# Kernel optimization log

Measured on AMD Instinct MI355X. Metric: run time of the kernel, lower is better.

Reference implementation:

```python
import jax, jax.numpy as jnp
import numpy as np

B, N, C = 4, 32768, 256
H, M = 8, 32
D = C // H


def _uni(k, shape, scale):
    return jax.random.uniform(k, shape, jnp.float32, -scale, scale)


def setup_inputs() -> dict:
    key = jax.random.key(0)
    ks = jax.random.split(key, 17)
    kc = 1.0 / np.sqrt(C).astype(np.float32)
    km = 1.0 / np.sqrt(H * M).astype(np.float32)
    inp = {}
    inp["x"] = jax.random.normal(ks[0], (B, N, C), jnp.float32)
    inp["latent_q"] = jax.random.normal(ks[1], (C, M), jnp.float32) * 0.1
    # k_proj ResidualMLP (num_layers=2)
    inp["k_fc1_w"] = _uni(ks[2], (C, C), kc); inp["k_fc1_b"] = _uni(ks[3], (C,), kc)
    inp["k_fcs_w"] = _uni(ks[4], (2, C, C), kc); inp["k_fcs_b"] = _uni(ks[5], (2, C), kc)
    inp["k_fc2_w"] = _uni(ks[6], (C, C), kc); inp["k_fc2_b"] = _uni(ks[7], (C,), kc)
    # v_proj ResidualMLP
    inp["v_fc1_w"] = _uni(ks[8], (C, C), kc); inp["v_fc1_b"] = _uni(ks[9], (C,), kc)
    inp["v_fcs_w"] = _uni(ks[10], (2, C, C), kc); inp["v_fcs_b"] = _uni(ks[11], (2, C), kc)
    inp["v_fc2_w"] = _uni(ks[12], (C, C), kc); inp["v_fc2_b"] = _uni(ks[13], (C,), kc)
    # head-cluster mixing 1x1 conv weight (H*M, H*M)
    inp["mix_w"] = _uni(ks[14], (H * M, H * M), km)
    inp["out_w"] = _uni(ks[15], (C, C), kc); inp["out_b"] = _uni(ks[16], (C,), kc)
    return inp


def _gelu(x):
    return jax.nn.gelu(x, approximate=False)  # torch nn.GELU default (erf)


def _rmlp(x, w1, b1, ws, bs, w2, b2):
    # ResidualMLP with input_residual=output_residual=True, num_layers=2
    h = x + _gelu(x @ w1.T + b1)
    for i in range(2):
        h = h + _gelu(h @ ws[i].T + bs[i])
    return h + (h @ w2.T + b2)


def reference(x, latent_q, k_fc1_w, k_fc1_b, k_fcs_w, k_fcs_b, k_fc2_w, k_fc2_b,
              v_fc1_w, v_fc1_b, v_fcs_w, v_fcs_b, v_fc2_w, v_fc2_b,
              mix_w, out_w, out_b):
    b, n, c = x.shape
    q = latent_q.reshape(H, M, D)                       # (C, M) -> (H, M, D)
    k = _rmlp(x, k_fc1_w, k_fc1_b, k_fcs_w, k_fcs_b, k_fc2_w, k_fc2_b)
    v = _rmlp(x, v_fc1_w, v_fc1_b, v_fcs_w, v_fcs_b, v_fc2_w, v_fc2_b)
    k = k.reshape(b, n, H, D).transpose(0, 2, 1, 3)     # b h n d
    v = v.reshape(b, n, H, D).transpose(0, 2, 1, 3)     # b h n d
    scores = jnp.einsum('hmd,bhnd->bhmn', q, k)         # (B,H,M,N)
    # 1x1 conv across flattened (H*M) channels == dense mix over head-cluster dim
    mixed = jnp.einsum('pq,bqn->bpn', mix_w, scores.reshape(b, H * M, n))
    mixed = mixed.reshape(b, H, M, n)
    enc = jax.nn.softmax(mixed, axis=-1)                # over N
    dec = jax.nn.softmax(mixed, axis=-2)                # over M
    z = jnp.einsum('bhmn,bhnd->bhmd', enc, v)           # encode to clusters
    o = jnp.einsum('bhmd,bhmn->bhnd', z, dec)           # decode to points
    o = o.transpose(0, 2, 1, 3).reshape(b, n, c)
    return o @ out_w.T + out_b
```

## Files before the change

### kernel.cpp

```cpp
#include <hip/hip_runtime.h>
#include <hip/hip_bf16.h>
#include <math.h>

#define BF16 __hip_bfloat16

typedef __bf16 bf16x8 __attribute__((ext_vector_type(8)));
typedef float  f32x4  __attribute__((ext_vector_type(4)));
typedef float  f32x16 __attribute__((ext_vector_type(16)));
typedef int    i32x4  __attribute__((ext_vector_type(4)));

__device__ inline float gelu_erf(float x) {
  float xs = x * 0.70710678118654752f;
  float a = fabsf(xs);
  float t = __builtin_amdgcn_rcpf(1.0f + 0.3275911f * a);
  float p = 1.061405429f;
  p = p * t - 1.453152027f;
  p = p * t + 1.421413741f;
  p = p * t - 0.284496736f;
  p = p * t + 0.254829592f;
  float e = __expf(-a * a);
  float y = 1.0f - p * t * e;
  float s = copysignf(y, xs);
  return 0.5f * x * (1.0f + s);
}

__device__ inline bf16x8 asbf8(i32x4 v) { union { i32x4 i; bf16x8 b; } u; u.i = v; return u.b; }

__device__ inline i32x4 aload16(const char* p) {
  i32x4 d;
  asm volatile("global_load_dwordx4 %0, %1, off" : "=v"(d) : "v"(p));
  return d;
}

template <int N> __device__ inline void vmwait() {
  if constexpr (N == 0)      asm volatile("s_waitcnt vmcnt(0)" ::: "memory");
  else if constexpr (N == 4) asm volatile("s_waitcnt vmcnt(4)" ::: "memory");
  else                       asm volatile("s_waitcnt vmcnt(8)" ::: "memory");
  __builtin_amdgcn_sched_barrier(0);
}

__device__ inline f32x4 ntload4(const float* p) {
  return __builtin_nontemporal_load((const f32x4*)p);
}
__device__ inline void ntstore4(float* p, f32x4 v) {
  __builtin_nontemporal_store(v, (f32x4*)p);
}

struct WPtrs { const float* p[9]; };
struct FArgs { const BF16* w[5]; const float* b[5]; };

__global__ void cast_w_kernel(WPtrs wp, BF16* __restrict__ out) {
  int i = blockIdx.x * 256 + threadIdx.x;
  int seg = i >> 16, d = i & 65535;
  int e = d & 7, lane = (d >> 3) & 63, kt = (d >> 9) & 7;
  int nc = (d >> 12) & 3, wc = (d >> 14) & 3;
  int fr = lane & 15, fq = lane >> 4;
  int row = wc * 64 + nc * 16 + fr, col = kt * 32 + fq * 8 + e;
  out[i] = __float2bfloat16(wp.p[seg][row * 256 + col]);
}

__global__ void build_wtilde(const float* __restrict__ mixw, const float* __restrict__ lq,
                             BF16* __restrict__ wt) {
  int p = blockIdx.x, c = threadIdx.x;
  int h = c >> 5, d = c & 31;
  float s = 0.f;
#pragma unroll
  for (int j = 0; j < 32; ++j)
    s += mixw[p * 256 + h * 32 + j] * lq[(h * 32 + j) * 32 + d];
  int wc = p >> 6, nc = (p >> 4) & 3, fr = p & 15;
  int kt = c >> 5, fq = (c >> 3) & 3, e = c & 7;
  int dst = ((((wc * 4 + nc) * 8 + kt) * 64) + (fq * 16 + fr)) * 8 + e;
  wt[dst] = __float2bfloat16(s);
}

__device__ inline void issue4(i32x4 (&buf)[4], const char* wlane, int kt) {
#pragma unroll
  for (int nc = 0; nc < 4; ++nc)
    buf[nc] = aload16(wlane + (nc * 8 + kt) * 1024);
}

__device__ inline void loada4(bf16x8 (&dst)[4], const char* act, int kt, int fr, int fq) {
#pragma unroll
  for (int nr = 0; nr < 4; ++nr) {
    int r = nr * 16 + fr;
    dst[nr] = *(const bf16x8*)(act + r * 512 + ((kt * 64 + fq * 16) ^ ((r & 7) << 4)));
  }
}

__device__ inline void mfma16w(f32x4 (&acc)[4][4], const i32x4 (&wbuf)[4], const bf16x8 (&af)[4]) {
#pragma unroll
  for (int nr = 0; nr < 4; ++nr)
#pragma unroll
    for (int nc = 0; nc < 4; ++nc)
      acc[nr][nc] = __builtin_amdgcn_mfma_f32_16x16x32_bf16(asbf8(wbuf[nc]), af[nr], acc[nr][nc], 0, 0, 0);
}

__device__ inline void kloop8(f32x4 (&acc)[4][4], const char* wlane, const char* act,
                              int fr, int fq) {
  i32x4 wb0[4], wb1[4], wb2[4];
  bf16x8 afA[4], afB[4];
  issue4(wb0, wlane, 0);
  issue4(wb1, wlane, 1);
  loada4(afA, act, 0, fr, fq);
  issue4(wb2, wlane, 2); loada4(afB, act, 1, fr, fq);
  vmwait<8>(); mfma16w(acc, wb0, afA);
  issue4(wb0, wlane, 3); loada4(afA, act, 2, fr, fq);
  vmwait<8>(); mfma16w(acc, wb1, afB);
  issue4(wb1, wlane, 4); loada4(afB, act, 3, fr, fq);
  vmwait<8>(); mfma16w(acc, wb2, afA);
  issue4(wb2, wlane, 5); loada4(afA, act, 4, fr, fq);
  vmwait<8>(); mfma16w(acc, wb0, afB);
  issue4(wb0, wlane, 6); loada4(afB, act, 5, fr, fq);
  vmwait<8>(); mfma16w(acc, wb1, afA);
  issue4(wb1, wlane, 7); loada4(afA, act, 6, fr, fq);
  vmwait<8>(); mfma16w(acc, wb2, afB);
  loada4(afB, act, 7, fr, fq);
  vmwait<4>(); mfma16w(acc, wb0, afA);
  vmwait<0>(); mfma16w(acc, wb1, afB);
}

__global__ __launch_bounds__(256, 3) void fused_k_mixed(
    const float* __restrict__ xin, FArgs args,
    float* __restrict__ mixed,
    float* __restrict__ pm, float* __restrict__ ps) {
  __shared__ __align__(16) char act[64 * 512];
  const int tid = threadIdx.x;
  const int blk = blockIdx.x;
  const int wc = tid >> 6, lane = tid & 63;
  const int fr = lane & 15, fq = lane >> 4;
  const size_t row0 = (size_t)blk * 64;

  {
    const float* xg = xin + row0 * 256;
#pragma unroll
    for (int rep = 0; rep < 16; ++rep) {
      int i = rep * 256 + tid;
      int r = i >> 6, c4 = (i & 63) << 2;
      f32x4 v = ntload4(xg + r * 256 + c4);
      union { __bf16 h[4]; unsigned long long u; } p;
      p.h[0] = (__bf16)v[0]; p.h[1] = (__bf16)v[1];
      p.h[2] = (__bf16)v[2]; p.h[3] = (__bf16)v[3];
      int byte = r * 512 + ((c4 * 2) ^ ((r & 7) << 4));
      *(unsigned long long*)(act + byte) = p.u;
    }
  }
  __syncthreads();

#pragma unroll 1
  for (int L = 0; L < 5; ++L) {
    const char* wlane = (const char*)args.w[L] + (size_t)(wc * 2048 + lane) * 16;
    f32x4 acc[4][4];
#pragma unroll
    for (int nr = 0; nr < 4; ++nr)
#pragma unroll
      for (int nc = 0; nc < 4; ++nc)
#pragma unroll
        for (int j = 0; j < 4; ++j) acc[nr][nc][j] = 0.f;

    kloop8(acc, wlane, act, fr, fq);
    __syncthreads();

    if (L == 4) {
      float* mg = mixed + row0 * 256;
#pragma unroll
      for (int nc = 0; nc < 4; ++nc) {
#pragma unroll
        for (int nr = 0; nr < 4; ++nr) {
          f32x4 st = { acc[nr][nc][0], acc[nr][nc][1], acc[nr][nc][2], acc[nr][nc][3] };
          ntstore4(mg + (size_t)(nr * 16 + fr) * 256 + wc * 64 + nc * 16 + fq * 4, st);
        }
        float mx[4], sm[4];
#pragma unroll
        for (int jj = 0; jj < 4; ++jj) {
          float m0 = fmaxf(fmaxf(acc[0][nc][jj], acc[1][nc][jj]),
                           fmaxf(acc[2][nc][jj], acc[3][nc][jj]));
#pragma unroll
          for (int d = 1; d < 16; d <<= 1) m0 = fmaxf(m0, __shfl_xor(m0, d));
          float s0 = 0.f;
#pragma unroll
          for (int nr = 0; nr < 4; ++nr) s0 += __expf(acc[nr][nc][jj] - m0);
#pragma unroll
          for (int d = 1; d < 16; d <<= 1) s0 += __shfl_xor(s0, d);
          mx[jj] = m0; sm[jj] = s0;
        }
        if (fr == 0) {
          int col = wc * 64 + nc * 16 + fq * 4;
          *(float4*)(pm + (size_t)blk * 256 + col) = {mx[0], mx[1], mx[2], mx[3]};
          *(float4*)(ps + (size_t)blk * 256 + col) = {sm[0], sm[1], sm[2], sm[3]};
        }
      }
    } else {
      const float* bb = args.b[L];
#pragma unroll
      for (int nc = 0; nc < 4; ++nc) {
        float4 b4 = *(const float4*)(bb + wc * 64 + nc * 16 + fq * 4);
#pragma unroll
        for (int nr = 0; nr < 4; ++nr) {
          int r = nr * 16 + fr;
          int cb2 = wc * 128 + nc * 32 + fq * 8;
          int byte = r * 512 + (cb2 ^ ((r & 7) << 4));
          union { __bf16 h[4]; unsigned long long u; } res, w2;
          res.u = *(unsigned long long*)(act + byte);
          float o0 = acc[nr][nc][0] + b4.x;
          float o1 = acc[nr][nc][1] + b4.y;
          float o2 = acc[nr][nc][2] + b4.z;
          float o3 = acc[nr][nc][3] + b4.w;
          if (L < 3) { o0 = gelu_erf(o0); o1 = gelu_erf(o1);
                       o2 = gelu_erf(o2); o3 = gelu_erf(o3); }
          w2.h[0] = (__bf16)((float)res.h[0] + o0);
          w2.h[1] = (__bf16)((float)res.h[1] + o1);
          w2.h[2] = (__bf16)((float)res.h[2] + o2);
          w2.h[3] = (__bf16)((float)res.h[3] + o3);
          *(unsigned long long*)(act + byte) = w2.u;
        }
      }
      __syncthreads();
    }
  }
}

__global__ void softmax_merge(const float* __restrict__ pm, const float* __restrict__ ps,
                              float* __restrict__ Mf, float* __restrict__ Sf) {
  int b = blockIdx.x, t = threadIdx.x;
  const float* pmb = pm + (size_t)b * 512 * 256;
  const float* psb = ps + (size_t)b * 512 * 256;
  float m = -3.0e38f, s = 0.f;
  for (int c = 0; c < 512; ++c) {
    float m2 = pmb[c * 256 + t];
    float s2 = psb[c * 256 + t];
    float mn = fmaxf(m, m2);
    s = s * __expf(m - mn) + s2 * __expf(m2 - mn);
    m = mn;
  }
  Mf[b * 256 + t] = m;
  Sf[b * 256 + t] = 1.f / s;
}

__global__ __launch_bounds__(256, 3) void fused_v_z(
    const float* __restrict__ xin, FArgs args,
    const float* __restrict__ mixed, const float* __restrict__ Mf,
    BF16* __restrict__ zpart) {
  __shared__ __align__(16) char act[64 * 512];
  const int tid = threadIdx.x;
  const int blk = blockIdx.x;
  const int wc = tid >> 6, lane = tid & 63;
  const int fr = lane & 15, fq = lane >> 4;
  const size_t row0 = (size_t)blk * 64;

  {
    const float* xg = xin + row0 * 256;
#pragma unroll
    for (int rep = 0; rep < 16; ++rep) {
      int i = rep * 256 + tid;
      int r = i >> 6, c4 = (i & 63) << 2;
      f32x4 v = ntload4(xg + r * 256 + c4);
      union { __bf16 h[4]; unsigned long long u; } p;
      p.h[0] = (__bf16)v[0]; p.h[1] = (__bf16)v[1];
      p.h[2] = (__bf16)v[2]; p.h[3] = (__bf16)v[3];
      int byte = r * 512 + ((c4 * 2) ^ ((r & 7) << 4));
      *(unsigned long long*)(act + byte) = p.u;
    }
  }
  __syncthreads();

#pragma unroll 1
  for (int L = 0; L < 4; ++L) {
    const char* wlane = (const char*)args.w[L] + (size_t)(wc * 2048 + lane) * 16;
    f32x4 acc[4][4];
#pragma unroll
    for (int nr = 0; nr < 4; ++nr)
#pragma unroll
      for (int nc = 0; nc < 4; ++nc)
#pragma unroll
        for (int j = 0; j < 4; ++j) acc[nr][nc][j] = 0.f;

    kloop8(acc, wlane, act, fr, fq);
    __syncthreads();

    const float* bb = args.b[L];
#pragma unroll
    for (int nc = 0; nc < 4; ++nc) {
      float4 b4 = *(const float4*)(bb + wc * 64 + nc * 16 + fq * 4);
#pragma unroll
      for (int nr = 0; nr < 4; ++nr) {
        int r = nr * 16 + fr;
        int cb2 = wc * 128 + nc * 32 + fq * 8;
        int byte = r * 512 + (cb2 ^ ((r & 7) << 4));
        union { __bf16 h[4]; unsigned long long u; } res, w2;
        res.u = *(unsigned long long*)(act + byte);
        float o0 = acc[nr][nc][0] + b4.x;
        float o1 = acc[nr][nc][1] + b4.y;
        float o2 = acc[nr][nc][2] + b4.z;
        float o3 = acc[nr][nc][3] + b4.w;
        if (L < 3) { o0 = gelu_erf(o0); o1 = gelu_erf(o1);
                     o2 = gelu_erf(o2); o3 = gelu_erf(o3); }
        w2.h[0] = (__bf16)((float)res.h[0] + o0);
        w2.h[1] = (__bf16)((float)res.h[1] + o1);
        w2.h[2] = (__bf16)((float)res.h[2] + o2);
        w2.h[3] = (__bf16)((float)res.h[3] + o3);
        *(unsigned long long*)(act + byte) = w2.u;
      }
    }
    __syncthreads();
  }

  const int l31 = lane & 31, kh = lane >> 5;
  const int b = (int)(row0 >> 15);
  for (int hi = 0; hi < 2; ++hi) {
    int h = wc * 2 + hi;
    int col = h * 32 + l31;
    float Mp = Mf[b * 256 + col];
    f32x16 zacc;
#pragma unroll
    for (int r = 0; r < 16; ++r) zacc[r] = 0.f;
#pragma unroll
    for (int s = 0; s < 4; ++s) {
      bf16x8 ea, vb;
      int rl0 = s * 16 + kh * 8;
      size_t nbase = row0 + rl0;
#pragma unroll
      for (int j = 0; j < 8; ++j) {
        float xv = __expf(mixed[(nbase + j) * 256 + col] - Mp);
        ea[j] = (__bf16)xv;
        int rl = rl0 + j;
        vb[j] = *(const __bf16*)(act + rl * 512 + ((col * 2) ^ ((rl & 7) << 4)));
      }
      zacc = __builtin_amdgcn_mfma_f32_32x32x16_bf16(ea, vb, zacc, 0, 0, 0);
    }
    BF16* zp = zpart + (size_t)blk * 8192 + h * 1024;
#pragma unroll
    for (int reg = 0; reg < 16; ++reg) {
      int m = (reg & 3) + 8 * (reg >> 2) + 4 * kh;
      zp[m * 32 + l31] = __float2bfloat16(zacc[reg]);
    }
  }
}

__global__ void z_merge(const BF16* __restrict__ zpart, const float* __restrict__ Sf,
                        float* __restrict__ z) {
  int i = blockIdx.x * 256 + threadIdx.x;
  int b = i >> 13, j = i & 8191;
  int p = j >> 5;
  float s = 0.f;
  for (int c = 0; c < 512; ++c)
    s += __bfloat162float(zpart[((size_t)(b * 512 + c)) * 8192 + j]);
  z[i] = s * Sf[b * 256 + p];
}

__global__ __launch_bounds__(256, 3) void decode_final(
    const float* __restrict__ mixed, const float* __restrict__ z,
    const BF16* __restrict__ wfin, const float* __restrict__ bias,
    float* __restrict__ fout) {
  __shared__ __align__(16) char act[64 * 512];
  const int tid = threadIdx.x, blk = blockIdx.x;
  const int wid = tid >> 6, lane = tid & 63;
  const int l31 = lane & 31, kh = lane >> 5;
  const int fr = lane & 15, fq = lane >> 4;
  const size_t row0 = (size_t)blk * 64;
  const int b = (int)(row0 >> 15);

  for (int hi = 0; hi < 2; ++hi) {
    int h = (wid << 1) + hi;
    bf16x8 zf[2];
#pragma unroll
    for (int ks = 0; ks < 2; ++ks)
#pragma unroll
      for (int j = 0; j < 8; ++j)
        zf[ks][j] = (__bf16)z[b * 8192 + h * 1024 + (ks * 16 + kh * 8 + j) * 32 + l31];
#pragma unroll 1
    for (int s = 0; s < 2; ++s) {
      size_t n = row0 + s * 32 + l31;
      const float* mrow = mixed + n * 256 + h * 32;
      float xv[16];
#pragma unroll
      for (int ks = 0; ks < 2; ++ks) {
        float4 a  = *(const float4*)(mrow + ks * 16 + kh * 8);
        float4 c4 = *(const float4*)(mrow + ks * 16 + kh * 8 + 4);
        xv[ks * 8 + 0] = a.x;  xv[ks * 8 + 1] = a.y;  xv[ks * 8 + 2] = a.z;  xv[ks * 8 + 3] = a.w;
        xv[ks * 8 + 4] = c4.x; xv[ks * 8 + 5] = c4.y; xv[ks * 8 + 6] = c4.z; xv[ks * 8 + 7] = c4.w;
      }
      float mx = xv[0];
#pragma unroll
      for (int i = 1; i < 16; ++i) mx = fmaxf(mx, xv[i]);
      mx = fmaxf(mx, __shfl_xor(mx, 32));
      float sm = 0.f, ev[16];
#pragma unroll
      for (int i = 0; i < 16; ++i) { ev[i] = __expf(xv[i] - mx); sm += ev[i]; }
      sm += __shfl_xor(sm, 32);
      float inv = 1.f / sm;
      bf16x8 af[2];
#pragma unroll
      for (int ks = 0; ks < 2; ++ks)
#pragma unroll
        for (int j = 0; j < 8; ++j) af[ks][j] = (__bf16)(ev[ks * 8 + j] * inv);
      f32x16 acc;
#pragma unroll
      for (int r = 0; r < 16; ++r) acc[r] = 0.f;
      acc = __builtin_amdgcn_mfma_f32_32x32x16_bf16(af[0], zf[0], acc, 0, 0, 0);
      acc = __builtin_amdgcn_mfma_f32_32x32x16_bf16(af[1], zf[1], acc, 0, 0, 0);
#pragma unroll
      for (int reg = 0; reg < 16; ++reg) {
        int rl = s * 32 + (reg & 3) + 8 * (reg >> 2) + 4 * kh;
        int cb = (h * 32 + l31) * 2;
        *(__bf16*)(act + rl * 512 + (cb ^ ((rl & 7) << 4))) = (__bf16)acc[reg];
      }
    }
  }
  __syncthreads();

  const int wc = wid;
  const char* wlane = (const char*)wfin + (size_t)(wc * 2048 + lane) * 16;
  f32x4 acc[4][4];
#pragma unroll
  for (int nr = 0; nr < 4; ++nr)
#pragma unroll
    for (int nc = 0; nc < 4; ++nc)
#pragma unroll
      for (int j = 0; j < 4; ++j) acc[nr][nc][j] = 0.f;

  kloop8(acc, wlane, act, fr, fq);

  float* og = fout + row0 * 256;
#pragma unroll
  for (int nc = 0; nc < 4; ++nc) {
    float4 b4 = *(const float4*)(bias + wc * 64 + nc * 16 + fq * 4);
#pragma unroll
    for (int nr = 0; nr < 4; ++nr) {
      float4 st = { acc[nr][nc][0] + b4.x, acc[nr][nc][1] + b4.y,
                    acc[nr][nc][2] + b4.z, acc[nr][nc][3] + b4.w };
      *(float4*)(og + (size_t)(nr * 16 + fr) * 256 + wc * 64 + nc * 16 + fq * 4) = st;
    }
  }
}

extern "C" void kernel_launch(void* const* d_in, const int* in_sizes, int n_in,
                              void* d_out, int out_size, void* d_ws, size_t ws_size,
                              hipStream_t stream) {
  const float* x     = (const float*)d_in[0];
  const float* lq    = (const float*)d_in[1];
  const float* kfc1b = (const float*)d_in[3];
  const float* kfcsb = (const float*)d_in[5];
  const float* kfc2b = (const float*)d_in[7];
  const float* vfc1b = (const float*)d_in[9];
  const float* vfcsb = (const float*)d_in[11];
  const float* vfc2b = (const float*)d_in[13];
  const float* mixw  = (const float*)d_in[14];
  const float* outb  = (const float*)d_in[16];

  const int R = in_sizes[0] / 256;

  char* ws = (char*)d_ws;
  BF16*  wbf   = (BF16*)(ws);
  BF16*  wt    = (BF16*)(ws + 1179648);
  float* pm    = (float*)(ws + 1310720);
  float* ps    = (float*)(ws + 3407872);
  float* Mf    = (float*)(ws + 5505024);
  float* Sf    = (float*)(ws + 5509120);
  BF16*  zpart = (BF16*)(ws + 5513216);
  float* z     = (float*)(ws + 39067648);
  float* mixed = (float*)d_out;

  WPtrs wp = {{(const float*)d_in[2], (const float*)d_in[4], (const float*)d_in[4] + 65536,
               (const float*)d_in[6], (const float*)d_in[8], (const float*)d_in[10],
               (const float*)d_in[10] + 65536, (const float*)d_in[12], (const float*)d_in[15]}};
  cast_w_kernel<<<2304, 256, 0, stream>>>(wp, wbf);
  build_wtilde<<<256, 256, 0, stream>>>(mixw, lq, wt);

  const int G = R / 64;

  FArgs a1;
  a1.w[0] = wbf + 0;      a1.b[0] = kfc1b;
  a1.w[1] = wbf + 65536;  a1.b[1] = kfcsb;
  a1.w[2] = wbf + 131072; a1.b[2] = kfcsb + 256;
  a1.w[3] = wbf + 196608; a1.b[3] = kfc2b;
  a1.w[4] = wt;           a1.b[4] = nullptr;
  fused_k_mixed<<<G, 256, 0, stream>>>(x, a1, mixed, pm, ps);

  softmax_merge<<<4, 256, 0, stream>>>(pm, ps, Mf, Sf);

  FArgs a2;
  a2.w[0] = wbf + 262144; a2.b[0] = vfc1b;
  a2.w[1] = wbf + 327680; a2.b[1] = vfcsb;
  a2.w[2] = wbf + 393216; a2.b[2] = vfcsb + 256;
  a2.w[3] = wbf + 458752; a2.b[3] = vfc2b;
  a2.w[4] = nullptr;      a2.b[4] = nullptr;
  fused_v_z<<<G, 256, 0, stream>>>(x, a2, mixed, Mf, zpart);

  z_merge<<<128, 256, 0, stream>>>(zpart, Sf, z);

  decode_final<<<G, 256, 0, stream>>>(mixed, z, wbf + 524288, outb, (float*)d_out);
}
```

Before: 387.0 us.

## Double row tile to 128 in fused MLP kernels to halve weight reloads

The fused K/mixed and V/z kernels now process 128 rows per block instead of 64, with an 8x4 accumulator tile per wave and a reworked k-loop that loads 8 activation fragments per weight chunk. Each weight fetch is reused across twice as many rows, and there are half as many partial softmax and z results for the merge kernels to reduce. The cost is doubled LDS per block and more accumulator registers, so launch bounds drop to 2 blocks per CU and occupancy falls. The activation prefetch is no longer double-buffered, which may expose LDS latency.

Result: faster. 353.9 us (median of 2 runs) (-8.6%).

```diff
diff --git a/kernel.cpp b/kernel.cpp
--- a/kernel.cpp
+++ b/kernel.cpp
@@ -87,9 +87,25 @@
   }
 }
 
+__device__ inline void loada8(bf16x8 (&dst)[8], const char* act, int kt, int fr, int fq) {
+#pragma unroll
+  for (int nr = 0; nr < 8; ++nr) {
+    int r = nr * 16 + fr;
+    dst[nr] = *(const bf16x8*)(act + r * 512 + ((kt * 64 + fq * 16) ^ ((r & 7) << 4)));
+  }
+}
+
 __device__ inline void mfma16w(f32x4 (&acc)[4][4], const i32x4 (&wbuf)[4], const bf16x8 (&af)[4]) {
 #pragma unroll
   for (int nr = 0; nr < 4; ++nr)
+#pragma unroll
+    for (int nc = 0; nc < 4; ++nc)
+      acc[nr][nc] = __builtin_amdgcn_mfma_f32_16x16x32_bf16(asbf8(wbuf[nc]), af[nr], acc[nr][nc], 0, 0, 0);
+}
+
+__device__ inline void mfma32w(f32x4 (&acc)[8][4], const i32x4 (&wbuf)[4], const bf16x8 (&af)[8]) {
+#pragma unroll
+  for (int nr = 0; nr < 8; ++nr)
 #pragma unroll
     for (int nc = 0; nc < 4; ++nc)
       acc[nr][nc] = __builtin_amdgcn_mfma_f32_16x16x32_bf16(asbf8(wbuf[nc]), af[nr], acc[nr][nc], 0, 0, 0);
@@ -119,21 +135,45 @@
   vmwait<0>(); mfma16w(acc, wb1, afB);
 }
 
-__global__ __launch_bounds__(256, 3) void fused_k_mixed(
+__device__ inline void kloop8x(f32x4 (&acc)[8][4], const char* wlane, const char* act,
+                               int fr, int fq) {
+  i32x4 wb0[4], wb1[4], wb2[4];
+  bf16x8 af[8];
+  issue4(wb0, wlane, 0);
+  issue4(wb1, wlane, 1);
+  issue4(wb2, wlane, 2); loada8(af, act, 0, fr, fq);
+  vmwait<8>(); mfma32w(acc, wb0, af);
+  issue4(wb0, wlane, 3); loada8(af, act, 1, fr, fq);
+  vmwait<8>(); mfma32w(acc, wb1, af);
+  issue4(wb1, wlane, 4); loada8(af, act, 2, fr, fq);
+  vmwait<8>(); mfma32w(acc, wb2, af);
+  issue4(wb2, wlane, 5); loada8(af, act, 3, fr, fq);
+  vmwait<8>(); mfma32w(acc, wb0, af);
+  issue4(wb0, wlane, 6); loada8(af, act, 4, fr, fq);
+  vmwait<8>(); mfma32w(acc, wb1, af);
+  issue4(wb1, wlane, 7); loada8(af, act, 5, fr, fq);
+  vmwait<8>(); mfma32w(acc, wb2, af);
+  loada8(af, act, 6, fr, fq);
+  vmwait<4>(); mfma32w(acc, wb0, af);
+  loada8(af, act, 7, fr, fq);
+  vmwait<0>(); mfma32w(acc, wb1, af);
+}
+
+__global__ __launch_bounds__(256, 2) void fused_k_mixed(
     const float* __restrict__ xin, FArgs args,
     float* __restrict__ mixed,
     float* __restrict__ pm, float* __restrict__ ps) {
-  __shared__ __align__(16) char act[64 * 512];
+  __shared__ __align__(16) char act[128 * 512];
   const int tid = threadIdx.x;
   const int blk = blockIdx.x;
   const int wc = tid >> 6, lane = tid & 63;
   const int fr = lane & 15, fq = lane >> 4;
-  const size_t row0 = (size_t)blk * 64;
+  const size_t row0 = (size_t)blk * 128;
 
   {
     const float* xg = xin + row0 * 256;
 #pragma unroll
-    for (int rep = 0; rep < 16; ++rep) {
+    for (int rep = 0; rep < 32; ++rep) {
       int i = rep * 256 + tid;
       int r = i >> 6, c4 = (i & 63) << 2;
       f32x4 v = ntload4(xg + r * 256 + c4);
@@ -149,15 +189,15 @@
 #pragma unroll 1
   for (int L = 0; L < 5; ++L) {
     const char* wlane = (const char*)args.w[L] + (size_t)(wc * 2048 + lane) * 16;
-    f32x4 acc[4][4];
-#pragma unroll
-    for (int nr = 0; nr < 4; ++nr)
+    f32x4 acc[8][4];
+#pragma unroll
+    for (int nr = 0; nr < 8; ++nr)
 #pragma unroll
       for (int nc = 0; nc < 4; ++nc)
 #pragma unroll
         for (int j = 0; j < 4; ++j) acc[nr][nc][j] = 0.f;
 
-    kloop8(acc, wlane, act, fr, fq);
+    kloop8x(acc, wlane, act, fr, fq);
     __syncthreads();
 
     if (L == 4) {
@@ -165,20 +205,21 @@
 #pragma unroll
       for (int nc = 0; nc < 4; ++nc) {
 #pragma unroll
-        for (int nr = 0; nr < 4; ++nr) {
+        for (int nr = 0; nr < 8; ++nr) {
           f32x4 st = { acc[nr][nc][0], acc[nr][nc][1], acc[nr][nc][2], acc[nr][nc][3] };
           ntstore4(mg + (size_t)(nr * 16 + fr) * 256 + wc * 64 + nc * 16 + fq * 4, st);
         }
         float mx[4], sm[4];
 #pragma unroll
         for (int jj = 0; jj < 4; ++jj) {
-          float m0 = fmaxf(fmaxf(acc[0][nc][jj], acc[1][nc][jj]),
-                           fmaxf(acc[2][nc][jj], acc[3][nc][jj]));
+          float m0 = acc[0][nc][jj];
+#pragma unroll
+          for (int nr = 1; nr < 8; ++nr) m0 = fmaxf(m0, acc[nr][nc][jj]);
 #pragma unroll
           for (int d = 1; d < 16; d <<= 1) m0 = fmaxf(m0, __shfl_xor(m0, d));
           float s0 = 0.f;
 #pragma unroll
-          for (int nr = 0; nr < 4; ++nr) s0 += __expf(acc[nr][nc][jj] - m0);
+          for (int nr = 0; nr < 8; ++nr) s0 += __expf(acc[nr][nc][jj] - m0);
 #pragma unroll
           for (int d = 1; d < 16; d <<= 1) s0 += __shfl_xor(s0, d);
           mx[jj] = m0; sm[jj] = s0;
@@ -195,7 +236,7 @@
       for (int nc = 0; nc < 4; ++nc) {
         float4 b4 = *(const float4*)(bb + wc * 64 + nc * 16 + fq * 4);
 #pragma unroll
-        for (int nr = 0; nr < 4; ++nr) {
+        for (int nr = 0; nr < 8; ++nr) {
           int r = nr * 16 + fr;
           int cb2 = wc * 128 + nc * 32 + fq * 8;
           int byte = r * 512 + (cb2 ^ ((r & 7) << 4));
@@ -222,10 +263,10 @@
 __global__ void softmax_merge(const float* __restrict__ pm, const float* __restrict__ ps,
                               float* __restrict__ Mf, float* __restrict__ Sf) {
   int b = blockIdx.x, t = threadIdx.x;
-  const float* pmb = pm + (size_t)b * 512 * 256;
-  const float* psb = ps + (size_t)b * 512 * 256;
+  const float* pmb = pm + (size_t)b * 256 * 256;
+  const float* psb = ps + (size_t)b * 256 * 256;
   float m = -3.0e38f, s = 0.f;
-  for (int c = 0; c < 512; ++c) {
+  for (int c = 0; c < 256; ++c) {
     float m2 = pmb[c * 256 + t];
     float s2 = psb[c * 256 + t];
     float mn = fmaxf(m, m2);
@@ -236,21 +277,21 @@
   Sf[b * 256 + t] = 1.f / s;
 }
 
-__global__ __launch_bounds__(256, 3) void fused_v_z(
+__global__ __launch_bounds__(256, 2) void fused_v_z(
     const float* __restrict__ xin, FArgs args,
     const float* __restrict__ mixed, const float* __restrict__ Mf,
     BF16* __restrict__ zpart) {
-  __shared__ __align__(16) char act[64 * 512];
+  __shared__ __align__(16) char act[128 * 512];
   const int tid = threadIdx.x;
   const int blk = blockIdx.x;
   const int wc = tid >> 6, lane = tid & 63;
   const int fr = lane & 15, fq = lane >> 4;
-  const size_t row0 = (size_t)blk * 64;
+  const size_t row0 = (size_t)blk * 128;
 
   {
     const float* xg = xin + row0 * 256;
 #pragma unroll
-    for (int rep = 0; rep < 16; ++rep) {
+    for (int rep = 0; rep < 32; ++rep) {
       int i = rep * 256 + tid;
       int r = i >> 6, c4 = (i & 63) << 2;
       f32x4 v = ntload4(xg + r * 256 + c4);
@@ -266,15 +307,15 @@
 #pragma unroll 1
   for (int L = 0; L < 4; ++L) {
     const char* wlane = (const char*)args.w[L] + (size_t)(wc * 2048 + lane) * 16;
-    f32x4 acc[4][4];
-#pragma unroll
-    for (int nr = 0; nr < 4; ++nr)
+    f32x4 acc[8][4];
+#pragma unroll
+    for (int nr = 0; nr < 8; ++nr)
 #pragma unroll
       for (int nc = 0; nc < 4; ++nc)
 #pragma unroll
         for (int j = 0; j < 4; ++j) acc[nr][nc][j] = 0.f;
 
-    kloop8(acc, wlane, act, fr, fq);
+    kloop8x(acc, wlane, act, fr, fq);
     __syncthreads();
 
     const float* bb = args.b[L];
@@ -282,7 +323,7 @@
     for (int nc = 0; nc < 4; ++nc) {
       float4 b4 = *(const float4*)(bb + wc * 64 + nc * 16 + fq * 4);
 #pragma unroll
-      for (int nr = 0; nr < 4; ++nr) {
+      for (int nr = 0; nr < 8; ++nr) {
         int r = nr * 16 + fr;
         int cb2 = wc * 128 + nc * 32 + fq * 8;
         int byte = r * 512 + (cb2 ^ ((r & 7) << 4));
@@ -314,7 +355,7 @@
 #pragma unroll
     for (int r = 0; r < 16; ++r) zacc[r] = 0.f;
 #pragma unroll
-    for (int s = 0; s < 4; ++s) {
+    for (int s = 0; s < 8; ++s) {
       bf16x8 ea, vb;
       int rl0 = s * 16 + kh * 8;
       size_t nbase = row0 + rl0;
@@ -342,8 +383,8 @@
   int b = i >> 13, j = i & 8191;
   int p = j >> 5;
   float s = 0.f;
-  for (int c = 0; c < 512; ++c)
-    s += __bfloat162float(zpart[((size_t)(b * 512 + c)) * 8192 + j]);
+  for (int c = 0; c < 256; ++c)
+    s += __bfloat162float(zpart[((size_t)(b * 256 + c)) * 8192 + j]);
   z[i] = s * Sf[b * 256 + p];
 }
 
@@ -453,11 +494,11 @@
   BF16*  wbf   = (BF16*)(ws);
   BF16*  wt    = (BF16*)(ws + 1179648);
   float* pm    = (float*)(ws + 1310720);
-  float* ps    = (float*)(ws + 3407872);
-  float* Mf    = (float*)(ws + 5505024);
-  float* Sf    = (float*)(ws + 5509120);
-  BF16*  zpart = (BF16*)(ws + 5513216);
-  float* z     = (float*)(ws + 39067648);
+  float* ps    = (float*)(ws + 2359296);
+  float* Mf    = (float*)(ws + 3407872);
+  float* Sf    = (float*)(ws + 3411968);
+  BF16*  zpart = (BF16*)(ws + 3416064);
+  float* z     = (float*)(ws + 20193280);
   float* mixed = (float*)d_out;
 
   WPtrs wp = {{(const float*)d_in[2], (const float*)d_in[4], (const float*)d_in[4] + 65536,
@@ -466,7 +507,8 @@
   cast_w_kernel<<<2304, 256, 0, stream>>>(wp, wbf);
   build_wtilde<<<256, 256, 0, stream>>>(mixw, lq, wt);
 
-  const int G = R / 64;
+  const int G = R / 128;
+  const int G2 = R / 64;
 
   FArgs a1;
   a1.w[0] = wbf + 0;      a1.b[0] = kfc1b;
@@ -488,5 +530,5 @@
 
   z_merge<<<128, 256, 0, stream>>>(zpart, Sf, z);
 
-  decode_final<<<G, 256, 0, stream>>>(mixed, z, wbf + 524288, outb, (float*)d_out);
-}
+  decode_final<<<G2, 256, 0, stream>>>(mixed, z, wbf + 524288, outb, (float*)d_out);
+}
```
